# Performance work log

Hardware: AMD Instinct MI355X
Metric: run time of the kernel (lower is better)

The kernel has to match this reference:

```python
import jax, jax.numpy as jnp
import numpy as np

B, T, K = 512, 1024, 64


def setup_inputs() -> dict:
    key = jax.random.key(0)
    k1, k2, k3, k4, k5 = jax.random.split(key, 5)
    emissions = jax.random.normal(k1, (B, T, K), dtype=jnp.float32)
    tags = jax.random.randint(k2, (B, T), 0, K, dtype=jnp.int64)
    mask = jnp.ones((B, T), dtype=bool)
    transitions = jax.random.uniform(k3, (K, K), minval=-0.1, maxval=0.1, dtype=jnp.float32)
    start_transitions = jax.random.uniform(k4, (K,), minval=-0.1, maxval=0.1, dtype=jnp.float32)
    end_transitions = jax.random.uniform(k5, (K,), minval=-0.1, maxval=0.1, dtype=jnp.float32)
    return {
        "emissions": emissions,
        "transitions": transitions,
        "start_transitions": start_transitions,
        "end_transitions": end_transitions,
        "tags": tags,
        "mask": mask,
    }


def _compute_score(emissions, transitions, start_transitions, end_transitions, tags, mask):
    # emissions: (B,T,K), tags: (B,T), mask: (B,T) bool
    maskf = mask.astype(emissions.dtype)
    # emission scores at gold tags, all positions: (B,T)
    emit = jnp.take_along_axis(emissions, tags[:, :, None], axis=2)[:, :, 0]
    score = emit[:, 0] + start_transitions[tags[:, 0]]
    # transition scores between consecutive gold tags: (B,T-1)
    trans = transitions[tags[:, :-1], tags[:, 1:]]
    score = score + jnp.sum((emit[:, 1:] + trans) * maskf[:, 1:], axis=1)
    seq_lengths = jnp.sum(mask.astype(jnp.int32), axis=1) - 1  # (B,)
    last_tags = jnp.take_along_axis(tags, seq_lengths[:, None], axis=1)[:, 0]
    score = score + end_transitions[last_tags]
    return score


def _log_partition(emissions, transitions, start_transitions, end_transitions, mask):
    maskf = mask.astype(emissions.dtype)
    alpha0 = emissions[:, 0] + start_transitions[None, :]  # (B,K)

    def step(alpha, xs):
        emit_t, mask_t = xs  # (B,K), (B,)
        # inner: (B, K_prev, K_cur)
        inner = alpha[:, :, None] + transitions[None, :, :] + emit_t[:, None, :]
        new_alpha = jax.nn.logsumexp(inner, axis=1)
        m = mask_t[:, None]
        alpha = new_alpha * m + alpha * (1.0 - m)
        return alpha, None

    xs = (jnp.swapaxes(emissions[:, 1:], 0, 1), jnp.swapaxes(maskf[:, 1:], 0, 1))
    alpha, _ = jax.lax.scan(step, alpha0, xs)
    alpha = alpha + end_transitions[None, :]
    return jax.nn.logsumexp(alpha, axis=1)  # (B,)


def reference(emissions, transitions, start_transitions, end_transitions, tags, mask):
    numerator = _compute_score(emissions, transitions, start_transitions, end_transitions, tags, mask)
    denominator = _log_partition(emissions, transitions, start_transitions, end_transitions, mask)
    return jnp.mean(denominator - numerator)
```

## Files before the change

### kernel.cpp

```cpp
#include <hip/hip_runtime.h>


#define CRF_B 512
#define CRF_T 1024
#define CRF_K 64

#define SWZF(v, imm) \
  __int_as_float(__builtin_amdgcn_ds_swizzle(__float_as_int(v), (imm)))

__device__ __forceinline__ float red_add16(float x) {
#if __has_builtin(__builtin_amdgcn_permlane16_swap)
  auto r = __builtin_amdgcn_permlane16_swap(__float_as_int(x),
                                            __float_as_int(x), false, false);
  return __int_as_float(r[0]) + __int_as_float(r[1]);
#else
  return x + SWZF(x, 0x401F);
#endif
}
__device__ __forceinline__ float red_add32(float x) {
#if __has_builtin(__builtin_amdgcn_permlane32_swap)
  auto r = __builtin_amdgcn_permlane32_swap(__float_as_int(x),
                                            __float_as_int(x), false, false);
  return __int_as_float(r[0]) + __int_as_float(r[1]);
#else
  return x + __shfl_xor(x, 32, 64);
#endif
}

#define BAR()                                          \
  do {                                                 \
    asm volatile("s_waitcnt lgkmcnt(0)" ::: "memory"); \
    __builtin_amdgcn_s_barrier();                      \
  } while (0)

#define STEP(RB, WB, EV, APPLY, DOMAX)                                     \
  do {                                                                     \
    float2 wm2;                                                            \
    if (APPLY) wm2 = *(const float2*)wmax;        \
    const float4* up = (const float4*)&ubuf[RB][h << 5];                   \
    float4 u0 = up[0], u1 = up[1], u2 = up[2], u3 = up[3];                 \
    float4 u4 = up[4], u5 = up[5], u6 = up[6], u7 = up[7];                 \
    float xe = __expf(EV);                   \
    int ex = 0;                                                            \
    if (APPLY) {                                                           \
      float mm = fmaxf(wm2.x, wm2.y);                                      \
      (void)frexpf(mm, &ex);                                               \
      cexp += ex;                                                          \
    }                                                                      \
    float a0 = u0.x * ke[0], a1 = u0.y * ke[1];                            \
    float a2 = u0.z * ke[2], a3 = u0.w * ke[3];                            \
    a0 = fmaf(u1.x, ke[4], a0);   a1 = fmaf(u1.y, ke[5], a1);              \
    a2 = fmaf(u1.z, ke[6], a2);   a3 = fmaf(u1.w, ke[7], a3);              \
    a0 = fmaf(u2.x, ke[8], a0);   a1 = fmaf(u2.y, ke[9], a1);              \
    a2 = fmaf(u2.z, ke[10], a2);  a3 = fmaf(u2.w, ke[11], a3);             \
    a0 = fmaf(u3.x, ke[12], a0);  a1 = fmaf(u3.y, ke[13], a1);             \
    a2 = fmaf(u3.z, ke[14], a2);  a3 = fmaf(u3.w, ke[15], a3);             \
    a0 = fmaf(u4.x, ke[16], a0);  a1 = fmaf(u4.y, ke[17], a1);             \
    a2 = fmaf(u4.z, ke[18], a2);  a3 = fmaf(u4.w, ke[19], a3);             \
    a0 = fmaf(u5.x, ke[20], a0);  a1 = fmaf(u5.y, ke[21], a1);             \
    a2 = fmaf(u5.z, ke[22], a2);  a3 = fmaf(u5.w, ke[23], a3);             \
    a0 = fmaf(u6.x, ke[24], a0);  a1 = fmaf(u6.y, ke[25], a1);             \
    a2 = fmaf(u6.z, ke[26], a2);  a3 = fmaf(u6.w, ke[27], a3);             \
    a0 = fmaf(u7.x, ke[28], a0);  a1 = fmaf(u7.y, ke[29], a1);             \
    a2 = fmaf(u7.z, ke[30], a2);  a3 = fmaf(u7.w, ke[31], a3);             \
    float r = (a0 + a1) + (a2 + a3);                                       \
    r = red_add32(r);         \
    if (APPLY) r = ldexpf(r, -ex);                                         \
    float un = r * xe;                                                     \
    if (l < 32) ubuf[WB][j] = un;                                          \
    if (DOMAX && l == 0) wmax[w] = un;                                     \
    BAR();                                                                 \
    sv = un;                                                               \
  } while (0)

__global__ __launch_bounds__(128, 1) void crf_fused_kernel(
    const float* __restrict__ emissions, const float* __restrict__ transitions,
    const float* __restrict__ start_t, const float* __restrict__ end_t,
    const int* __restrict__ tags32, float* __restrict__ d_out) {
  __shared__ __align__(16) float ubuf[2][64];
  __shared__ __align__(8) float wmax[2];
  __shared__ float redS[2];
  __shared__ float redC[2];

  const int tid = threadIdx.x;
  const int w = tid >> 6;
  const int l = tid & 63;
  const int h = l >> 5;
  const int j = (w << 5) + (l & 31);
  const int b = blockIdx.x;

  float ke[32];
#pragma unroll
  for (int k = 0; k < 32; ++k)
    ke[k] = __expf(transitions[(32 * h + k) * CRF_K + j]);
#pragma unroll
  for (int k = 0; k < 32; ++k) asm volatile("" : "+v"(ke[k]));

  const float* eptr = emissions + (size_t)b * (CRF_T * CRF_K) + j;

  float u0i = __expf(eptr[0] + start_t[j]);
  if (l < 32) ubuf[0][j] = u0i;
  if (l == 0) wmax[w] = u0i;
  int cexp = 0;
  float sv = u0i;

  float ea[4], eb[4], ec[4];
#pragma unroll
  for (int k = 0; k < 4; ++k) ea[k] = eptr[(size_t)(1 + k) * CRF_K];
#pragma unroll
  for (int k = 0; k < 4; ++k) eb[k] = eptr[(size_t)(5 + k) * CRF_K];

  BAR();

  int t0 = 9;
  for (int gg = 0; gg < 85; ++gg) {
#pragma unroll
    for (int k = 0; k < 4; ++k) {
      int t = t0 + k;
      t = t < CRF_T ? t : CRF_T - 1;
      ec[k] = eptr[(size_t)t * CRF_K];
    }
    t0 += 4;
    STEP(0, 1, ea[0], true, false);
    STEP(1, 0, ea[1], false, false);
    STEP(0, 1, ea[2], false, false);
    STEP(1, 0, ea[3], false, true);
#pragma unroll
    for (int k = 0; k < 4; ++k) {
      int t = t0 + k;
      t = t < CRF_T ? t : CRF_T - 1;
      ea[k] = eptr[(size_t)t * CRF_K];
    }
    t0 += 4;
    STEP(0, 1, eb[0], true, false);
    STEP(1, 0, eb[1], false, false);
    STEP(0, 1, eb[2], false, false);
    STEP(1, 0, eb[3], false, true);
#pragma unroll
    for (int k = 0; k < 4; ++k) {
      int t = t0 + k;
      t = t < CRF_T ? t : CRF_T - 1;
      eb[k] = eptr[(size_t)t * CRF_K];
    }
    t0 += 4;
    STEP(0, 1, ec[0], true, false);
    STEP(1, 0, ec[1], false, false);
    STEP(0, 1, ec[2], false, false);
    STEP(1, 0, ec[3], false, true);
  }
  STEP(0, 1, ea[0], true, false);
  STEP(1, 0, ea[1], false, false);
  STEP(0, 1, ea[2], false, false);

  {
    float v = sv * __expf(end_t[j]);
    v += SWZF(v, 0x041F);
    v += SWZF(v, 0x081F);
    v += SWZF(v, 0x101F);
    v += SWZF(v, 0x201F);
    v = red_add16(v);
    if (l == 0) redS[w] = v;
  }

  int hv = tags32[2 * l + 1];
  unsigned long long any = __ballot(hv != 0);
  const int mult = (any == 0ULL) ? 2 : 1;
  const size_t tbase = (size_t)b * CRF_T;
  const float* ebase = emissions + (size_t)b * (CRF_T * CRF_K);

  float sacc = 0.f;
#pragma unroll
  for (int it = 0; it < 8; ++it) {
    const int t = tid + 128 * it;
    const int tg = tags32[(tbase + (size_t)t) * (size_t)mult];
    float c = ebase[(size_t)t * CRF_K + tg];
    if (t == 0)
      c += start_t[tg];
    else
      c += transitions[tags32[(tbase + (size_t)t - 1) * (size_t)mult] * CRF_K +
                       tg];
    if (t == CRF_T - 1) c += end_t[tg];
    sacc += c;
  }
  sacc += SWZF(sacc, 0x041F);
  sacc += SWZF(sacc, 0x081F);
  sacc += SWZF(sacc, 0x101F);
  sacc += SWZF(sacc, 0x201F);
  sacc = red_add32(red_add16(sacc));
  if (l == 0) redC[w] = sacc;

  __syncthreads();
  if (tid == 0) {
    float S = redS[0] + redS[1];
    float sc = redC[0] + redC[1];
    d_out[b] = (float)cexp * 0.69314718055994530942f + logf(S) - sc;
  }
}

__global__ __launch_bounds__(512) void crf_final_kernel(
    const float* __restrict__ d, float* __restrict__ out) {
  const int tid = threadIdx.x;
  float v = d[tid];
#pragma unroll
  for (int off = 32; off >= 1; off >>= 1) v += __shfl_xor(v, off, 64);
  __shared__ float red[8];
  if ((tid & 63) == 0) red[tid >> 6] = v;
  __syncthreads();
  if (tid == 0) {
    float s = 0.f;
#pragma unroll
    for (int i = 0; i < 8; ++i) s += red[i];
    out[0] = s * (1.0f / CRF_B);
  }
}

extern "C" void kernel_launch(void* const* d_in, const int* in_sizes, int n_in,
                              void* d_out, int out_size, void* d_ws,
                              size_t ws_size, hipStream_t stream) {
  const float* emissions   = (const float*)d_in[0];
  const float* transitions = (const float*)d_in[1];
  const float* start_t     = (const float*)d_in[2];
  const float* end_t       = (const float*)d_in[3];
  const int*   tags        = (const int*)d_in[4];

  float* out = (float*)d_out;
  float* d   = (float*)d_ws;

  crf_fused_kernel<<<CRF_B, 128, 0, stream>>>(emissions, transitions, start_t,
                                              end_t, tags, d);
  crf_final_kernel<<<1, 512, 0, stream>>>(d, out);
}
```

Measured before the change: 367.7 us.

## Run CRF forward recursion in one wavefront using DPP exchanges instead of LDS barriers

```diff
diff --git a/kernel.cpp b/kernel.cpp
--- a/kernel.cpp
+++ b/kernel.cpp
@@ -5,8 +5,19 @@
 #define CRF_T 1024
 #define CRF_K 64
 
+typedef float f32x4 __attribute__((ext_vector_type(4)));
+
 #define SWZF(v, imm) \
   __int_as_float(__builtin_amdgcn_ds_swizzle(__float_as_int(v), (imm)))
+
+#define DPPF(v, ctrl)                                                      \
+  __int_as_float(__builtin_amdgcn_mov_dpp(__float_as_int(v), (ctrl), 0xF,  \
+                                          0xF, true))
+#define CTL_X1 0xB1
+#define CTL_X2 0x4E
+#define CTL_X3 0x1B
+#define CTL_MIR 0x140
+#define CTL_HMIR 0x141
 
 __device__ __forceinline__ float red_add16(float x) {
 #if __has_builtin(__builtin_amdgcn_permlane16_swap)
@@ -27,93 +38,105 @@
 #endif
 }
 
-#define BAR()                                          \
-  do {                                                 \
-    asm volatile("s_waitcnt lgkmcnt(0)" ::: "memory"); \
-    __builtin_amdgcn_s_barrier();                      \
+#define PIN_KQ()                                                           \
+  asm volatile("" : "+v"(kq0), "+v"(kq1), "+v"(kq2), "+v"(kq3), "+v"(kq4), \
+                    "+v"(kq5), "+v"(kq6), "+v"(kq7), "+v"(kq8), "+v"(kq9), \
+                    "+v"(kq10), "+v"(kq11), "+v"(kq12), "+v"(kq13),        \
+                    "+v"(kq14), "+v"(kq15))
+
+#define FM(acc0, acc1, acc2, acc3, bm, kq)                                 \
+  acc0 = fmaf((bm), kq[0], acc0); acc1 = fmaf((bm), kq[1], acc1);          \
+  acc2 = fmaf((bm), kq[2], acc2); acc3 = fmaf((bm), kq[3], acc3)
+
+#define STEP(EV, APPLY, DOMAX)                                             \
+  do {                                                                     \
+    if (APPLY) sv = ldexpf(sv, -exs);                                      \
+    float t1 = DPPF(sv, CTL_X1), t2 = DPPF(sv, CTL_X2);                    \
+    float t3 = DPPF(sv, CTL_X3);                                           \
+    float t7 = DPPF(sv, CTL_HMIR), tF = DPPF(sv, CTL_MIR);                 \
+    float t4 = DPPF(t7, CTL_X3), t5 = DPPF(t7, CTL_X2);                    \
+    float t6 = DPPF(t7, CTL_X1), t8 = DPPF(t7, CTL_MIR);                   \
+    float tC = DPPF(tF, CTL_X3), tD = DPPF(tF, CTL_X2);                    \
+    float tE = DPPF(tF, CTL_X1);                                           \
+    float t9 = DPPF(t8, CTL_X1), tA = DPPF(t8, CTL_X2);                    \
+    float tB = DPPF(t8, CTL_X3);                                           \
+    float xe = __expf(EV);                                                 \
+    float a0 = sv * kq0[0], a1 = sv * kq0[1];                              \
+    float a2 = sv * kq0[2], a3 = sv * kq0[3];                              \
+    float b0 = t1 * kq1[0], b1 = t1 * kq1[1];                              \
+    float b2 = t1 * kq1[2], b3 = t1 * kq1[3];                              \
+    FM(a0, a1, a2, a3, t2, kq2);   FM(b0, b1, b2, b3, t3, kq3);            \
+    FM(a0, a1, a2, a3, t4, kq4);   FM(b0, b1, b2, b3, t5, kq5);            \
+    FM(a0, a1, a2, a3, t6, kq6);   FM(b0, b1, b2, b3, t7, kq7);            \
+    FM(a0, a1, a2, a3, t8, kq8);   FM(b0, b1, b2, b3, t9, kq9);            \
+    FM(a0, a1, a2, a3, tA, kq10);  FM(b0, b1, b2, b3, tB, kq11);           \
+    FM(a0, a1, a2, a3, tC, kq12);  FM(b0, b1, b2, b3, tD, kq13);           \
+    FM(a0, a1, a2, a3, tE, kq14);  FM(b0, b1, b2, b3, tF, kq15);           \
+    a0 += b0; a1 += b1; a2 += b2; a3 += b3;                                \
+    a0 = red_add32(red_add16(a0));                                         \
+    a1 = red_add32(red_add16(a1));                                         \
+    a2 = red_add32(red_add16(a2));                                         \
+    a3 = red_add32(red_add16(a3));                                         \
+    float red = q == 0 ? a0 : q == 1 ? a1 : q == 2 ? a2 : a3;              \
+    sv = red * xe;                                                         \
+    if (DOMAX) {                                                           \
+      int exl;                                                             \
+      (void)frexpf(sv, &exl);                                              \
+      exs = __builtin_amdgcn_readfirstlane(exl);                           \
+      cexp += exs;                                                         \
+    }                                                                      \
   } while (0)
 
-#define STEP(RB, WB, EV, APPLY, DOMAX)                                     \
-  do {                                                                     \
-    float2 wm2;                                                            \
-    if (APPLY) wm2 = *(const float2*)wmax;        \
-    const float4* up = (const float4*)&ubuf[RB][h << 5];                   \
-    float4 u0 = up[0], u1 = up[1], u2 = up[2], u3 = up[3];                 \
-    float4 u4 = up[4], u5 = up[5], u6 = up[6], u7 = up[7];                 \
-    float xe = __expf(EV);                   \
-    int ex = 0;                                                            \
-    if (APPLY) {                                                           \
-      float mm = fmaxf(wm2.x, wm2.y);                                      \
-      (void)frexpf(mm, &ex);                                               \
-      cexp += ex;                                                          \
-    }                                                                      \
-    float a0 = u0.x * ke[0], a1 = u0.y * ke[1];                            \
-    float a2 = u0.z * ke[2], a3 = u0.w * ke[3];                            \
-    a0 = fmaf(u1.x, ke[4], a0);   a1 = fmaf(u1.y, ke[5], a1);              \
-    a2 = fmaf(u1.z, ke[6], a2);   a3 = fmaf(u1.w, ke[7], a3);              \
-    a0 = fmaf(u2.x, ke[8], a0);   a1 = fmaf(u2.y, ke[9], a1);              \
-    a2 = fmaf(u2.z, ke[10], a2);  a3 = fmaf(u2.w, ke[11], a3);             \
-    a0 = fmaf(u3.x, ke[12], a0);  a1 = fmaf(u3.y, ke[13], a1);             \
-    a2 = fmaf(u3.z, ke[14], a2);  a3 = fmaf(u3.w, ke[15], a3);             \
-    a0 = fmaf(u4.x, ke[16], a0);  a1 = fmaf(u4.y, ke[17], a1);             \
-    a2 = fmaf(u4.z, ke[18], a2);  a3 = fmaf(u4.w, ke[19], a3);             \
-    a0 = fmaf(u5.x, ke[20], a0);  a1 = fmaf(u5.y, ke[21], a1);             \
-    a2 = fmaf(u5.z, ke[22], a2);  a3 = fmaf(u5.w, ke[23], a3);             \
-    a0 = fmaf(u6.x, ke[24], a0);  a1 = fmaf(u6.y, ke[25], a1);             \
-    a2 = fmaf(u6.z, ke[26], a2);  a3 = fmaf(u6.w, ke[27], a3);             \
-    a0 = fmaf(u7.x, ke[28], a0);  a1 = fmaf(u7.y, ke[29], a1);             \
-    a2 = fmaf(u7.z, ke[30], a2);  a3 = fmaf(u7.w, ke[31], a3);             \
-    float r = (a0 + a1) + (a2 + a3);                                       \
-    r = red_add32(r);         \
-    if (APPLY) r = ldexpf(r, -ex);                                         \
-    float un = r * xe;                                                     \
-    if (l < 32) ubuf[WB][j] = un;                                          \
-    if (DOMAX && l == 0) wmax[w] = un;                                     \
-    BAR();                                                                 \
-    sv = un;                                                               \
-  } while (0)
-
-__global__ __launch_bounds__(128, 1) void crf_fused_kernel(
+__global__ void __attribute__((amdgpu_flat_work_group_size(64, 64)))
+__attribute__((amdgpu_waves_per_eu(1, 1))) crf_fused_kernel(
     const float* __restrict__ emissions, const float* __restrict__ transitions,
     const float* __restrict__ start_t, const float* __restrict__ end_t,
     const int* __restrict__ tags32, float* __restrict__ d_out) {
-  __shared__ __align__(16) float ubuf[2][64];
-  __shared__ __align__(8) float wmax[2];
-  __shared__ float redS[2];
-  __shared__ float redC[2];
-
-  const int tid = threadIdx.x;
-  const int w = tid >> 6;
-  const int l = tid & 63;
-  const int h = l >> 5;
-  const int j = (w << 5) + (l & 31);
+  const int l = threadIdx.x;
+  const int q = l >> 4;
+  const int r = l & 15;
   const int b = blockIdx.x;
 
-  float ke[32];
-#pragma unroll
-  for (int k = 0; k < 32; ++k)
-    ke[k] = __expf(transitions[(32 * h + k) * CRF_K + j]);
-#pragma unroll
-  for (int k = 0; k < 32; ++k) asm volatile("" : "+v"(ke[k]));
-
-  const float* eptr = emissions + (size_t)b * (CRF_T * CRF_K) + j;
-
-  float u0i = __expf(eptr[0] + start_t[j]);
-  if (l < 32) ubuf[0][j] = u0i;
-  if (l == 0) wmax[w] = u0i;
-  int cexp = 0;
-  float sv = u0i;
+  f32x4 kq0, kq1, kq2, kq3, kq4, kq5, kq6, kq7;
+  f32x4 kq8, kq9, kq10, kq11, kq12, kq13, kq14, kq15;
+  {
+    const float* tb = transitions;
+#define LK(vec, m)                                                   \
+  do {                                                               \
+    const float* row = tb + (16 * q + (r ^ (m))) * CRF_K + r;        \
+    vec[0] = __expf(row[0]);                                         \
+    vec[1] = __expf(row[16]);                                        \
+    vec[2] = __expf(row[32]);                                        \
+    vec[3] = __expf(row[48]);                                        \
+  } while (0)
+    LK(kq0, 0);  LK(kq1, 1);  LK(kq2, 2);  LK(kq3, 3);
+    LK(kq4, 4);  LK(kq5, 5);  LK(kq6, 6);  LK(kq7, 7);
+    LK(kq8, 8);  LK(kq9, 9);  LK(kq10, 10); LK(kq11, 11);
+    LK(kq12, 12); LK(kq13, 13); LK(kq14, 14); LK(kq15, 15);
+#undef LK
+  }
+  PIN_KQ();
+
+  const float* eptr = emissions + (size_t)b * (CRF_T * CRF_K) + l;
+
+  float sv = __expf(eptr[0] + start_t[l]);
+  int exs, cexp = 0;
+  {
+    int exl;
+    (void)frexpf(sv, &exl);
+    exs = __builtin_amdgcn_readfirstlane(exl);
+    cexp += exs;
+  }
 
   float ea[4], eb[4], ec[4];
 #pragma unroll
   for (int k = 0; k < 4; ++k) ea[k] = eptr[(size_t)(1 + k) * CRF_K];
 #pragma unroll
   for (int k = 0; k < 4; ++k) eb[k] = eptr[(size_t)(5 + k) * CRF_K];
-
-  BAR();
 
   int t0 = 9;
   for (int gg = 0; gg < 85; ++gg) {
+    PIN_KQ();
 #pragma unroll
     for (int k = 0; k < 4; ++k) {
       int t = t0 + k;
@@ -121,10 +144,10 @@
       ec[k] = eptr[(size_t)t * CRF_K];
     }
     t0 += 4;
-    STEP(0, 1, ea[0], true, false);
-    STEP(1, 0, ea[1], false, false);
-    STEP(0, 1, ea[2], false, false);
-    STEP(1, 0, ea[3], false, true);
+    STEP(ea[0], true, false);
+    STEP(ea[1], false, false);
+    STEP(ea[2], false, false);
+    STEP(ea[3], false, true);
 #pragma unroll
     for (int k = 0; k < 4; ++k) {
       int t = t0 + k;
@@ -132,10 +155,10 @@
       ea[k] = eptr[(size_t)t * CRF_K];
     }
     t0 += 4;
-    STEP(0, 1, eb[0], true, false);
-    STEP(1, 0, eb[1], false, false);
-    STEP(0, 1, eb[2], false, false);
-    STEP(1, 0, eb[3], false, true);
+    STEP(eb[0], true, false);
+    STEP(eb[1], false, false);
+    STEP(eb[2], false, false);
+    STEP(eb[3], false, true);
 #pragma unroll
     for (int k = 0; k < 4; ++k) {
       int t = t0 + k;
@@ -143,24 +166,22 @@
       eb[k] = eptr[(size_t)t * CRF_K];
     }
     t0 += 4;
-    STEP(0, 1, ec[0], true, false);
-    STEP(1, 0, ec[1], false, false);
-    STEP(0, 1, ec[2], false, false);
-    STEP(1, 0, ec[3], false, true);
-  }
-  STEP(0, 1, ea[0], true, false);
-  STEP(1, 0, ea[1], false, false);
-  STEP(0, 1, ea[2], false, false);
-
-  {
-    float v = sv * __expf(end_t[j]);
-    v += SWZF(v, 0x041F);
-    v += SWZF(v, 0x081F);
-    v += SWZF(v, 0x101F);
-    v += SWZF(v, 0x201F);
-    v = red_add16(v);
-    if (l == 0) redS[w] = v;
-  }
+    STEP(ec[0], true, false);
+    STEP(ec[1], false, false);
+    STEP(ec[2], false, false);
+    STEP(ec[3], false, true);
+  }
+  STEP(ea[0], true, false);
+  STEP(ea[1], false, false);
+  STEP(ea[2], false, false);
+
+  float v = sv * __expf(end_t[l]);
+  v += SWZF(v, 0x041F);
+  v += SWZF(v, 0x081F);
+  v += SWZF(v, 0x101F);
+  v += SWZF(v, 0x201F);
+  v = red_add32(red_add16(v));
+  const float logZ = (float)cexp * 0.69314718055994530942f + logf(v);
 
   int hv = tags32[2 * l + 1];
   unsigned long long any = __ballot(hv != 0);
@@ -170,8 +191,8 @@
 
   float sacc = 0.f;
 #pragma unroll
-  for (int it = 0; it < 8; ++it) {
-    const int t = tid + 128 * it;
+  for (int it = 0; it < 16; ++it) {
+    const int t = l + 64 * it;
     const int tg = tags32[(tbase + (size_t)t) * (size_t)mult];
     float c = ebase[(size_t)t * CRF_K + tg];
     if (t == 0)
@@ -187,14 +208,8 @@
   sacc += SWZF(sacc, 0x101F);
   sacc += SWZF(sacc, 0x201F);
   sacc = red_add32(red_add16(sacc));
-  if (l == 0) redC[w] = sacc;
-
-  __syncthreads();
-  if (tid == 0) {
-    float S = redS[0] + redS[1];
-    float sc = redC[0] + redC[1];
-    d_out[b] = (float)cexp * 0.69314718055994530942f + logf(S) - sc;
-  }
+
+  if (l == 0) d_out[b] = logZ - sacc;
 }
 
 __global__ __launch_bounds__(512) void crf_final_kernel(
@@ -226,7 +241,7 @@
   float* out = (float*)d_out;
   float* d   = (float*)d_ws;
 
-  crf_fused_kernel<<<CRF_B, 128, 0, stream>>>(emissions, transitions, start_t,
-                                              end_t, tags, d);
+  crf_fused_kernel<<<CRF_B, 64, 0, stream>>>(emissions, transitions, start_t,
+                                             end_t, tags, d);
   crf_final_kernel<<<1, 512, 0, stream>>>(d, out);
 }
```

New measurement: 394.1 us. 7.2% more time.
